# Kernel optimization log

Measured on AMD Instinct MI355X. Metric: run time of the kernel, lower is better.

## Reference

```python
import jax, jax.numpy as jnp
import numpy as np

D = 512
K = 14            # 13 anomaly classes + 1 normal
NORMAL_IDX = K - 1
ALPHA = 0.2       # PLG alpha
THETA = 0.55      # PLG threshold
EPS = 1e-8


def _minmax(x, axis):
    mn = jnp.min(x, axis=axis, keepdims=True)
    mx = jnp.max(x, axis=axis, keepdims=True)
    return (x - mn) / (mx - mn + EPS)


def setup_inputs() -> dict:
    key = jax.random.key(0)
    k1, k2, k3, k4, k5 = jax.random.split(key, 5)
    B_n, B_a, F = 16, 16, 4096
    normal_feats = jax.random.normal(k1, (B_n, F, D), dtype=jnp.float32)
    anomaly_feats = jax.random.normal(k2, (B_a, F, D), dtype=jnp.float32)
    anomaly_class_idx = jax.random.randint(k3, (B_a,), 0, K - 1)  # in [0, K-2]
    # learned text prompt embeddings (output of PromptTextEncoder, pre-normalization)
    T_emb = jax.random.normal(k4, (K, D), dtype=jnp.float32)
    # stand-in temporal scoring head (TCSAL replaced by linear head; see notes)
    w_score = jax.random.normal(k5, (D,), dtype=jnp.float32) / np.sqrt(D)
    b_score = jnp.zeros((), dtype=jnp.float32)
    return {"normal_feats": normal_feats, "anomaly_feats": anomaly_feats,
            "anomaly_class_idx": anomaly_class_idx, "T_emb": T_emb,
            "w_score": w_score, "b_score": b_score}


def reference(normal_feats, anomaly_feats, anomaly_class_idx, T_emb, w_score, b_score):
    B_a, F_a, _ = anomaly_feats.shape
    # L2-normalized text embeddings (K, D)
    T = T_emb / (jnp.linalg.norm(T_emb, axis=-1, keepdims=True) + EPS)
    T_anomaly = T[:NORMAL_IDX]          # (K-1, D)
    T_n = T[NORMAL_IDX]                 # (D,)  use_nvp=False -> T_n_enhanced = T_n
    T_n_enhanced = T_n

    # dense similarities
    S_nn = jnp.einsum('bfd,d->bf', normal_feats, T_n_enhanced)      # (B_n, F_n)
    phi_na = jnp.einsum('bfd,kd->bfk', normal_feats, T_anomaly)     # (B_n, F_n, K-1)
    S_an = jnp.einsum('bfd,d->bf', anomaly_feats, T_n_enhanced)     # (B_a, F_a)

    # per-sample true-class gather + matmul (vectorized: gather class vec then contract)
    T_true = T_anomaly[anomaly_class_idx]                            # (B_a, D)
    S_aa_true = jnp.einsum('bfd,bd->bf', anomaly_feats, T_true)      # (B_a, F_a)

    # 'other classes' similarities: exclude tau[b] per sample.
    # Since exactly one class is excluded, max_other = K-2 statically.
    phi_all = jnp.einsum('bfd,kd->bfk', anomaly_feats, T_anomaly)    # (B_a, F_a, K-1)
    j = jnp.arange(K - 2)                                            # (K-2,)
    other_idx = jnp.where(j[None, :] < anomaly_class_idx[:, None], j[None, :], j[None, :] + 1)  # (B_a, K-2)
    phi_aa_other = jnp.take_along_axis(
        phi_all, jnp.broadcast_to(other_idx[:, None, :], (B_a, F_a, K - 2)), axis=2)

    # pseudo-label generator (alpha-fused, normality-guided, thresholded)
    s_aa = _minmax(S_aa_true, axis=1)
    s_an = _minmax(S_an, axis=1)
    fused = (1.0 - ALPHA) * s_aa + ALPHA * (1.0 - s_an)
    pseudo_labels = (fused > THETA).astype(jnp.float32)

    # temporal scores (linear head stand-in for TCSAL)
    scores = jax.nn.sigmoid(jnp.einsum('bfd,d->bf', anomaly_feats, w_score) + b_score)

    S_aa_norm = _minmax(S_aa_true, axis=1)
    return (S_nn, phi_na, S_an, S_aa_true, phi_aa_other, S_aa_norm,
            pseudo_labels, scores, T_n_enhanced)
```

## Files before the change

kernel.cpp:

```cpp
#include <hip/hip_runtime.h>
#include <math.h>

#define D 512
#define K 14
#define EPS 1e-8f
#define NROWS 65536

#define O_SNN       0
#define O_PHINA     65536
#define O_SAN       917504
#define O_SAA       983040
#define O_PHIOTHER  1048576
#define O_SAANORM   1835008
#define O_PSEUDO    1900544
#define O_SCORES    1966080
#define O_TN        2031616

__device__ __forceinline__ float wave_sum(float v) {
    v += __shfl_xor(v, 1);
    v += __shfl_xor(v, 2);
    v += __shfl_xor(v, 4);
    v += __shfl_xor(v, 8);
    v += __shfl_xor(v, 16);
    v += __shfl_xor(v, 32);
    return v;
}
__device__ __forceinline__ float wave_min(float v) {
    v = fminf(v, __shfl_xor(v, 1));
    v = fminf(v, __shfl_xor(v, 2));
    v = fminf(v, __shfl_xor(v, 4));
    v = fminf(v, __shfl_xor(v, 8));
    v = fminf(v, __shfl_xor(v, 16));
    v = fminf(v, __shfl_xor(v, 32));
    return v;
}
__device__ __forceinline__ float wave_max(float v) {
    v = fmaxf(v, __shfl_xor(v, 1));
    v = fmaxf(v, __shfl_xor(v, 2));
    v = fmaxf(v, __shfl_xor(v, 4));
    v = fmaxf(v, __shfl_xor(v, 8));
    v = fmaxf(v, __shfl_xor(v, 16));
    v = fmaxf(v, __shfl_xor(v, 32));
    return v;
}

__device__ __forceinline__ float multi_reduce16(float (&vals)[16], int lane) {
#pragma unroll
    for (int s = 0; s < 4; s++) {
        const int half = 8 >> s;
        const bool sel = (lane >> s) & 1;
#pragma unroll
        for (int i = 0; i < half; i++) {
            float lo = vals[i], hi = vals[i + half];
            float a = sel ? lo : hi;
            float b = __shfl_xor(a, 1 << s);
            vals[i] = sel ? (hi + b) : (lo + b);
        }
    }
    float v = vals[0];
    v += __shfl_xor(v, 16);
    v += __shfl_xor(v, 32);
    return v;
}

__device__ __forceinline__ int bitrev4(int x) {
    return ((x & 1) << 3) | ((x & 2) << 1) | ((x & 4) >> 1) | ((x & 8) >> 3);
}

__global__ __launch_bounds__(64) void kprep(const float* __restrict__ T_emb,
                                            const float* __restrict__ w_score,
                                            float* __restrict__ W,
                                            float* __restrict__ tn_out) {
    int lane = threadIdx.x;
    int w = blockIdx.x;
    float4* W4 = (float4*)W;
    if (w < K) {
        const float4* src = (const float4*)T_emb + w * 128;
        float4 a = src[lane];
        float4 b = src[64 + lane];
        float ss = a.x * a.x + a.y * a.y + a.z * a.z + a.w * a.w
                 + b.x * b.x + b.y * b.y + b.z * b.z + b.w * b.w;
        ss = wave_sum(ss);
        float inv = 1.0f / (sqrtf(ss) + EPS);
        float4 na = make_float4(a.x * inv, a.y * inv, a.z * inv, a.w * inv);
        float4 nb = make_float4(b.x * inv, b.y * inv, b.z * inv, b.w * inv);
        W4[w * 128 + lane] = na;
        W4[w * 128 + 64 + lane] = nb;
        if (w == K - 1) {
            float4* t4 = (float4*)tn_out;
            t4[lane] = na;
            t4[64 + lane] = nb;
        }
    } else {
        const float4* src = (const float4*)w_score;
        W4[14 * 128 + lane] = src[lane];
        W4[14 * 128 + 64 + lane] = src[64 + lane];
    }
}

template <int NK>
__device__ __forceinline__ void dotvals(float (&vals)[16],
                                        const float4 f0, const float4 f1,
                                        const float4 (&t0)[NK], const float4 (&t1)[NK]) {
#pragma unroll
    for (int k = 0; k < NK; k++) {
        float s = f0.x * t0[k].x;
        s = fmaf(f0.y, t0[k].y, s);
        s = fmaf(f0.z, t0[k].z, s);
        s = fmaf(f0.w, t0[k].w, s);
        s = fmaf(f1.x, t1[k].x, s);
        s = fmaf(f1.y, t1[k].y, s);
        s = fmaf(f1.z, t1[k].z, s);
        s = fmaf(f1.w, t1[k].w, s);
        vals[k] = s;
    }
#pragma unroll
    for (int k = NK; k < 16; k++) vals[k] = 0.0f;
}

template <bool ANOM>
__device__ __forceinline__ void finish_row(float (&vals)[16], int row, int lane, int myk,
                                           const int* __restrict__ cls, float bsc,
                                           float* __restrict__ S_nn, float* __restrict__ phi_na,
                                           float* __restrict__ S_an, float* __restrict__ S_aa,
                                           float* __restrict__ phi_other, float* __restrict__ scores) {
    float v = multi_reduce16(vals, lane);
    if (ANOM) {
        if (lane < 16 && myk < 15) {
            int ci = cls[row >> 12];
            float val = v;
            float* ptr;
            if (myk < 13) {
                ptr = (myk == ci) ? (S_aa + row)
                                  : (phi_other + row * 12 + ((myk < ci) ? myk : myk - 1));
            } else if (myk == 13) {
                ptr = S_an + row;
            } else {
                ptr = scores + row;
                val = 1.0f / (1.0f + expf(-(v + bsc)));
            }
            *ptr = val;
        }
    } else {
        if (lane < 16 && myk < 14) {
            float* ptr = (myk < 13) ? (phi_na + row * 13 + myk) : (S_nn + row);
            *ptr = v;
        }
    }
}

template <bool ANOM>
__device__ __forceinline__ void run_half(const float4* __restrict__ feats,
                                         const float4* __restrict__ W4,
                                         const int* __restrict__ cls, float bsc,
                                         int wave, int nw, int lane, int myk,
                                         float* __restrict__ S_nn, float* __restrict__ phi_na,
                                         float* __restrict__ S_an, float* __restrict__ S_aa,
                                         float* __restrict__ phi_other, float* __restrict__ scores) {
    constexpr int NK = ANOM ? 15 : 14;
    float4 t0[NK], t1[NK];
#pragma unroll
    for (int k = 0; k < NK; k++) {
        t0[k] = W4[k * 128 + lane];
        t1[k] = W4[k * 128 + 64 + lane];
    }

    int pA = wave;
    int pB = wave + nw;
    int pC = wave + 2 * nw;

    float4 A0 = feats[pA * 128 + lane];
    float4 A1 = feats[pA * 128 + 64 + lane];
    float4 B0 = feats[pB * 128 + lane];
    float4 B1 = feats[pB * 128 + 64 + lane];
    float valsA[16], valsB[16];
    dotvals<NK>(valsA, A0, A1, t0, t1);

    const int niter = NROWS / nw;
#pragma unroll 1
    for (int it = 0; it < (niter - 2) / 2; ++it) {
        A0 = feats[pC * 128 + lane];
        A1 = feats[pC * 128 + 64 + lane];
        dotvals<NK>(valsB, B0, B1, t0, t1);
        finish_row<ANOM>(valsA, pA, lane, myk, cls, bsc, S_nn, phi_na, S_an, S_aa, phi_other, scores);
        pA = pB; pB = pC; pC += nw;
        B0 = feats[pC * 128 + lane];
        B1 = feats[pC * 128 + 64 + lane];
        dotvals<NK>(valsA, A0, A1, t0, t1);
        finish_row<ANOM>(valsB, pA, lane, myk, cls, bsc, S_nn, phi_na, S_an, S_aa, phi_other, scores);
        pA = pB; pB = pC; pC += nw;
    }
    dotvals<NK>(valsB, B0, B1, t0, t1);
    finish_row<ANOM>(valsA, pA, lane, myk, cls, bsc, S_nn, phi_na, S_an, S_aa, phi_other, scores);
    finish_row<ANOM>(valsB, pB, lane, myk, cls, bsc, S_nn, phi_na, S_an, S_aa, phi_other, scores);
}

__global__ __launch_bounds__(256, 2) void kmain(const float4* __restrict__ nf,
                                                const float4* __restrict__ af,
                                                const float4* __restrict__ W4,
                                                const int* __restrict__ cls,
                                                const float* __restrict__ b_score,
                                                float* __restrict__ S_nn,
                                                float* __restrict__ phi_na,
                                                float* __restrict__ S_an,
                                                float* __restrict__ S_aa,
                                                float* __restrict__ phi_other,
                                                float* __restrict__ scores) {
    int lane = threadIdx.x & 63;
    int half = gridDim.x >> 1;
    int nw = half << 2;
    bool anom = (int)blockIdx.x >= half;
    int bid = anom ? (int)blockIdx.x - half : (int)blockIdx.x;
    int wave = (bid << 2) + (threadIdx.x >> 6);
    int myk = bitrev4(lane);
    float bsc = *b_score;
    if (anom)
        run_half<true>(af, W4, cls, bsc, wave, nw, lane, myk,
                       S_nn, phi_na, S_an, S_aa, phi_other, scores);
    else
        run_half<false>(nf, W4, cls, bsc, wave, nw, lane, myk,
                        S_nn, phi_na, S_an, S_aa, phi_other, scores);
}

__global__ __launch_bounds__(256) void kpost(const float* __restrict__ S_aa,
                                             const float* __restrict__ S_an,
                                             float* __restrict__ S_aa_norm,
                                             float* __restrict__ pseudo) {
    int b = blockIdx.x;
    int t = threadIdx.x;
    int lane = t & 63, wid = t >> 6;
    const float* pa = S_aa + b * 4096;
    const float* pn = S_an + b * 4096;
    float a[16], n[16];
    float mnA = 1e30f, mxA = -1e30f, mnN = 1e30f, mxN = -1e30f;
#pragma unroll
    for (int i = 0; i < 16; i++) {
        a[i] = pa[t + i * 256];
        n[i] = pn[t + i * 256];
        mnA = fminf(mnA, a[i]); mxA = fmaxf(mxA, a[i]);
        mnN = fminf(mnN, n[i]); mxN = fmaxf(mxN, n[i]);
    }
    mnA = wave_min(mnA); mxA = wave_max(mxA);
    mnN = wave_min(mnN); mxN = wave_max(mxN);
    __shared__ float red[4][4];
    if (lane == 0) {
        red[wid][0] = mnA; red[wid][1] = mxA;
        red[wid][2] = mnN; red[wid][3] = mxN;
    }
    __syncthreads();
    mnA = fminf(fminf(red[0][0], red[1][0]), fminf(red[2][0], red[3][0]));
    mxA = fmaxf(fmaxf(red[0][1], red[1][1]), fmaxf(red[2][1], red[3][1]));
    mnN = fminf(fminf(red[0][2], red[1][2]), fminf(red[2][2], red[3][2]));
    mxN = fmaxf(fmaxf(red[0][3], red[1][3]), fmaxf(red[2][3], red[3][3]));
    float dA = mxA - mnA + EPS;
    float dN = mxN - mnN + EPS;
#pragma unroll
    for (int i = 0; i < 16; i++) {
        float s_aa = (a[i] - mnA) / dA;
        float s_an = (n[i] - mnN) / dN;
        float fused = 0.8f * s_aa + 0.2f * (1.0f - s_an);
        pseudo[b * 4096 + t + i * 256] = fused > 0.55f ? 1.0f : 0.0f;
        S_aa_norm[b * 4096 + t + i * 256] = s_aa;
    }
}

extern "C" void kernel_launch(void* const* d_in, const int* in_sizes, int n_in,
                              void* d_out, int out_size, void* d_ws, size_t ws_size,
                              hipStream_t stream) {
    const float* normal_feats  = (const float*)d_in[0];
    const float* anomaly_feats = (const float*)d_in[1];
    const int*   cls           = (const int*)d_in[2];
    const float* T_emb         = (const float*)d_in[3];
    const float* w_score       = (const float*)d_in[4];
    const float* b_score       = (const float*)d_in[5];
    float* out = (float*)d_out;

    float* W = (float*)d_ws;

    kprep<<<15, 64, 0, stream>>>(T_emb, w_score, W, out + O_TN);

    kmain<<<2048, 256, 0, stream>>>((const float4*)normal_feats,
                                    (const float4*)anomaly_feats,
                                    (const float4*)W, cls, b_score,
                                    out + O_SNN, out + O_PHINA, out + O_SAN, out + O_SAA,
                                    out + O_PHIOTHER, out + O_SCORES);

    kpost<<<16, 256, 0, stream>>>(out + O_SAA, out + O_SAN,
                                  out + O_SAANORM, out + O_PSEUDO);
}
```

Baseline: 361.7 us.

## Split main kernel per half and stage weight vectors in shared memory

Replaces the single fused kernel, which held all class vectors in registers, with two templated launches (normal and anomaly), each caching the weight vectors in LDS. Register pressure drops, so launch bounds can request 4 blocks per SM instead of 2 for higher occupancy to hide HBM latency. The pipelining becomes a simple one-row prefetch. The cost is LDS reads on every dot product and an extra launch boundary between the two halves.

```diff
diff --git a/kernel.cpp b/kernel.cpp
--- a/kernel.cpp
+++ b/kernel.cpp
@@ -98,128 +98,82 @@
     }
 }
 
-template <int NK>
-__device__ __forceinline__ void dotvals(float (&vals)[16],
-                                        const float4 f0, const float4 f1,
-                                        const float4 (&t0)[NK], const float4 (&t1)[NK]) {
-#pragma unroll
-    for (int k = 0; k < NK; k++) {
-        float s = f0.x * t0[k].x;
-        s = fmaf(f0.y, t0[k].y, s);
-        s = fmaf(f0.z, t0[k].z, s);
-        s = fmaf(f0.w, t0[k].w, s);
-        s = fmaf(f1.x, t1[k].x, s);
-        s = fmaf(f1.y, t1[k].y, s);
-        s = fmaf(f1.z, t1[k].z, s);
-        s = fmaf(f1.w, t1[k].w, s);
-        vals[k] = s;
-    }
-#pragma unroll
-    for (int k = NK; k < 16; k++) vals[k] = 0.0f;
-}
-
 template <bool ANOM>
-__device__ __forceinline__ void finish_row(float (&vals)[16], int row, int lane, int myk,
-                                           const int* __restrict__ cls, float bsc,
-                                           float* __restrict__ S_nn, float* __restrict__ phi_na,
-                                           float* __restrict__ S_an, float* __restrict__ S_aa,
-                                           float* __restrict__ phi_other, float* __restrict__ scores) {
-    float v = multi_reduce16(vals, lane);
-    if (ANOM) {
-        if (lane < 16 && myk < 15) {
-            int ci = cls[row >> 12];
-            float val = v;
-            float* ptr;
-            if (myk < 13) {
-                ptr = (myk == ci) ? (S_aa + row)
-                                  : (phi_other + row * 12 + ((myk < ci) ? myk : myk - 1));
-            } else if (myk == 13) {
-                ptr = S_an + row;
-            } else {
-                ptr = scores + row;
-                val = 1.0f / (1.0f + expf(-(v + bsc)));
+__global__ __launch_bounds__(256, 4) void kdot(const float4* __restrict__ feats,
+                                               const float4* __restrict__ W4,
+                                               const int* __restrict__ cls,
+                                               const float* __restrict__ b_score,
+                                               float* __restrict__ S_nn,
+                                               float* __restrict__ phi_na,
+                                               float* __restrict__ S_an,
+                                               float* __restrict__ S_aa,
+                                               float* __restrict__ phi_other,
+                                               float* __restrict__ scores) {
+    constexpr int NK = ANOM ? 15 : 14;
+    __shared__ float4 Wl[NK * 128];
+
+    for (int i = threadIdx.x; i < NK * 128; i += 256) Wl[i] = W4[i];
+    __syncthreads();
+
+    int lane = threadIdx.x & 63;
+    int wave = (blockIdx.x * 256 + threadIdx.x) >> 6;
+    int nw = (gridDim.x * 256) >> 6;
+    const int myk = bitrev4(lane);
+    float bsc = ANOM ? *b_score : 0.0f;
+
+    int row = wave;
+    float4 f0 = feats[row * 128 + lane];
+    float4 f1 = feats[row * 128 + 64 + lane];
+    while (row < NROWS) {
+        int nrow = row + nw;
+        float4 g0, g1;
+        if (nrow < NROWS) {
+            g0 = feats[nrow * 128 + lane];
+            g1 = feats[nrow * 128 + 64 + lane];
+        }
+        float vals[16];
+#pragma unroll
+        for (int k = 0; k < NK; k++) {
+            float4 w0 = Wl[k * 128 + lane];
+            float4 w1 = Wl[k * 128 + 64 + lane];
+            float s = f0.x * w0.x;
+            s = fmaf(f0.y, w0.y, s);
+            s = fmaf(f0.z, w0.z, s);
+            s = fmaf(f0.w, w0.w, s);
+            s = fmaf(f1.x, w1.x, s);
+            s = fmaf(f1.y, w1.y, s);
+            s = fmaf(f1.z, w1.z, s);
+            s = fmaf(f1.w, w1.w, s);
+            vals[k] = s;
+        }
+#pragma unroll
+        for (int k = NK; k < 16; k++) vals[k] = 0.0f;
+
+        float v = multi_reduce16(vals, lane);
+        if (ANOM) {
+            if (lane < 16 && myk < 15) {
+                int ci = cls[row >> 12];
+                float val = v;
+                float* ptr;
+                if (myk < 13) {
+                    ptr = (myk == ci) ? (S_aa + row)
+                                      : (phi_other + row * 12 + ((myk < ci) ? myk : myk - 1));
+                } else if (myk == 13) {
+                    ptr = S_an + row;
+                } else {
+                    ptr = scores + row;
+                    val = 1.0f / (1.0f + expf(-(v + bsc)));
+                }
+                *ptr = val;
             }
-            *ptr = val;
-        }
-    } else {
-        if (lane < 16 && myk < 14) {
-            float* ptr = (myk < 13) ? (phi_na + row * 13 + myk) : (S_nn + row);
-            *ptr = v;
-        }
-    }
-}
-
-template <bool ANOM>
-__device__ __forceinline__ void run_half(const float4* __restrict__ feats,
-                                         const float4* __restrict__ W4,
-                                         const int* __restrict__ cls, float bsc,
-                                         int wave, int nw, int lane, int myk,
-                                         float* __restrict__ S_nn, float* __restrict__ phi_na,
-                                         float* __restrict__ S_an, float* __restrict__ S_aa,
-                                         float* __restrict__ phi_other, float* __restrict__ scores) {
-    constexpr int NK = ANOM ? 15 : 14;
-    float4 t0[NK], t1[NK];
-#pragma unroll
-    for (int k = 0; k < NK; k++) {
-        t0[k] = W4[k * 128 + lane];
-        t1[k] = W4[k * 128 + 64 + lane];
-    }
-
-    int pA = wave;
-    int pB = wave + nw;
-    int pC = wave + 2 * nw;
-
-    float4 A0 = feats[pA * 128 + lane];
-    float4 A1 = feats[pA * 128 + 64 + lane];
-    float4 B0 = feats[pB * 128 + lane];
-    float4 B1 = feats[pB * 128 + 64 + lane];
-    float valsA[16], valsB[16];
-    dotvals<NK>(valsA, A0, A1, t0, t1);
-
-    const int niter = NROWS / nw;
-#pragma unroll 1
-    for (int it = 0; it < (niter - 2) / 2; ++it) {
-        A0 = feats[pC * 128 + lane];
-        A1 = feats[pC * 128 + 64 + lane];
-        dotvals<NK>(valsB, B0, B1, t0, t1);
-        finish_row<ANOM>(valsA, pA, lane, myk, cls, bsc, S_nn, phi_na, S_an, S_aa, phi_other, scores);
-        pA = pB; pB = pC; pC += nw;
-        B0 = feats[pC * 128 + lane];
-        B1 = feats[pC * 128 + 64 + lane];
-        dotvals<NK>(valsA, A0, A1, t0, t1);
-        finish_row<ANOM>(valsB, pA, lane, myk, cls, bsc, S_nn, phi_na, S_an, S_aa, phi_other, scores);
-        pA = pB; pB = pC; pC += nw;
-    }
-    dotvals<NK>(valsB, B0, B1, t0, t1);
-    finish_row<ANOM>(valsA, pA, lane, myk, cls, bsc, S_nn, phi_na, S_an, S_aa, phi_other, scores);
-    finish_row<ANOM>(valsB, pB, lane, myk, cls, bsc, S_nn, phi_na, S_an, S_aa, phi_other, scores);
-}
-
-__global__ __launch_bounds__(256, 2) void kmain(const float4* __restrict__ nf,
-                                                const float4* __restrict__ af,
-                                                const float4* __restrict__ W4,
-                                                const int* __restrict__ cls,
-                                                const float* __restrict__ b_score,
-                                                float* __restrict__ S_nn,
-                                                float* __restrict__ phi_na,
-                                                float* __restrict__ S_an,
-                                                float* __restrict__ S_aa,
-                                                float* __restrict__ phi_other,
-                                                float* __restrict__ scores) {
-    int lane = threadIdx.x & 63;
-    int half = gridDim.x >> 1;
-    int nw = half << 2;
-    bool anom = (int)blockIdx.x >= half;
-    int bid = anom ? (int)blockIdx.x - half : (int)blockIdx.x;
-    int wave = (bid << 2) + (threadIdx.x >> 6);
-    int myk = bitrev4(lane);
-    float bsc = *b_score;
-    if (anom)
-        run_half<true>(af, W4, cls, bsc, wave, nw, lane, myk,
-                       S_nn, phi_na, S_an, S_aa, phi_other, scores);
-    else
-        run_half<false>(nf, W4, cls, bsc, wave, nw, lane, myk,
-                        S_nn, phi_na, S_an, S_aa, phi_other, scores);
+        } else {
+            if (lane < 16 && myk < 14) {
+                float* ptr = (myk < 13) ? (phi_na + row * 13 + myk) : (S_nn + row);
+                *ptr = v;
+            }
+        }
+        row = nrow; f0 = g0; f1 = g1;
+    }
 }
 
 __global__ __launch_bounds__(256) void kpost(const float* __restrict__ S_aa,
@@ -279,11 +233,16 @@
 
     kprep<<<15, 64, 0, stream>>>(T_emb, w_score, W, out + O_TN);
 
-    kmain<<<2048, 256, 0, stream>>>((const float4*)normal_feats,
-                                    (const float4*)anomaly_feats,
-                                    (const float4*)W, cls, b_score,
-                                    out + O_SNN, out + O_PHINA, out + O_SAN, out + O_SAA,
-                                    out + O_PHIOTHER, out + O_SCORES);
+    kdot<false><<<1024, 256, 0, stream>>>((const float4*)normal_feats,
+                                          (const float4*)W, nullptr, b_score,
+                                          out + O_SNN, out + O_PHINA,
+                                          nullptr, nullptr, nullptr, nullptr);
+
+    kdot<true><<<1024, 256, 0, stream>>>((const float4*)anomaly_feats,
+                                         (const float4*)W, cls, b_score,
+                                         nullptr, nullptr,
+                                         out + O_SAN, out + O_SAA,
+                                         out + O_PHIOTHER, out + O_SCORES);
 
     kpost<<<16, 256, 0, stream>>>(out + O_SAA, out + O_SAN,
                                   out + O_SAANORM, out + O_PSEUDO);
```

Measured after the change: 492.2 us. 36.1% more time.
